# Performance work log

Measured on AMD Instinct MI355X. Metric: run time of the kernel, lower is better.

The kernel has to match this reference:

```python
import jax, jax.numpy as jnp
import numpy as np

H, D = 8, 32  # heads, head_dim
EPS = 1e-5    # torch LayerNorm default eps


def setup_inputs() -> dict:
    key = jax.random.key(0)
    ks = jax.random.split(key, 4)
    B, N, C = 2, 2048, 256
    inner = H * D
    return {
        "node_features": jax.random.normal(ks[0], (B, N, C), jnp.float32),
        "ln_gamma": jnp.ones((C,), jnp.float32),
        "ln_beta": jnp.zeros((C,), jnp.float32),
        "W_qkv": jax.random.normal(ks[1], (3 * inner, C), jnp.float32) * 0.02,
        "W_gate": jax.random.normal(ks[2], (inner, C), jnp.float32) * 0.02,
        "b_gate": jnp.ones((inner,), jnp.float32),
        "W_final": jax.random.normal(ks[3], (C, inner), jnp.float32) * 0.02,
        "b_final": jnp.zeros((C,), jnp.float32),
    }


def reference(node_features, ln_gamma, ln_beta, W_qkv, W_gate, b_gate, W_final, b_final):
    x = node_features                                   # [B, N, C]
    B, N, _ = x.shape

    # LayerNorm (biased variance, as in torch.nn.LayerNorm)
    mu = jnp.mean(x, axis=-1, keepdims=True)
    var = jnp.mean(jnp.square(x - mu), axis=-1, keepdims=True)
    normed = (x - mu) / jnp.sqrt(var + EPS) * ln_gamma + ln_beta

    # Fused QKV projection (no bias), split into heads: [B, H, N, D]
    qkv = normed @ W_qkv.T                              # [B, N, 3*H*D]
    q, k, v = jnp.split(qkv, 3, axis=-1)

    def to_heads(t):
        return t.reshape(B, N, H, D).transpose(0, 2, 1, 3)

    q, k, v = to_heads(q), to_heads(k), to_heads(v)

    # Gate is computed from the UN-normalized input
    gate = jax.nn.sigmoid(to_heads(x @ W_gate.T + b_gate))  # [B, H, N, D]

    scores = jnp.einsum('bhid,bhjd->bhij', q, k) * (D ** -0.5)
    attn = jax.nn.softmax(scores, axis=-1)              # softmax over j

    # NOTE: non-standard contraction over i (attn^T @ V), output indexed by j
    out = jnp.einsum('bhij,bhid->bhjd', attn, v) * gate  # [B, H, N, D]
    out = out.transpose(0, 2, 1, 3).reshape(B, N, H * D)

    return x + out @ W_final.T + b_final
```

## Files before the change

kernel.cpp:

```cpp
#include <hip/hip_runtime.h>
#include <math.h>

#define Bb 2
#define Nn 2048
#define Cc 256
#define Hh 8
#define Dd 32
#define INNER 256
#define TQKV 768
#define NROWS 4096
#define EPSf 1e-5f
#define SCALEf 0.17677669529663687f

typedef unsigned short u16;
typedef short s16x8 __attribute__((ext_vector_type(8)));
typedef float f32x4 __attribute__((ext_vector_type(4)));
#define MFMA16 __builtin_amdgcn_mfma_f32_16x16x32_bf16

#define OFF_NORMED 0u
#define OFF_MPART  0u
#define OFF_LPART  65536u
#define OFF_VTGHI  0u
#define OFF_VTGLO  524288u
#define OFF_AOHI   0u
#define OFF_AOLO   524288u
#define OFF_GATE   1048576u
#define OFF_MM     2097152u
#define OFF_QHI    2129920u
#define OFF_QLO    3702784u
#define OFF_WHI    5275648u
#define OFF_WLO    5439488u
#define OFF_P1     5603328u

__device__ inline u16 f2bf(float f) {
  union { float f; unsigned u; } v; v.f = f;
  unsigned r = v.u + 0x7fffu + ((v.u >> 16) & 1u);
  return (u16)(r >> 16);
}
__device__ inline float bf2f(u16 h) {
  union { unsigned u; float f; } v; v.u = ((unsigned)h) << 16;
  return v.f;
}

__global__ __launch_bounds__(256) void ln_kernel(
    const float* __restrict__ x, const float* __restrict__ gam,
    const float* __restrict__ bet, float* __restrict__ normed) {
  int row = blockIdx.x;
  int tid = threadIdx.x;
  size_t base = (size_t)row * Cc;
  float v = x[base + tid];
  float s1 = v, s2 = v * v;
  #pragma unroll
  for (int off = 32; off; off >>= 1) {
    s1 += __shfl_xor(s1, off);
    s2 += __shfl_xor(s2, off);
  }
  __shared__ float w1[4], w2[4];
  if ((tid & 63) == 0) { w1[tid >> 6] = s1; w2[tid >> 6] = s2; }
  __syncthreads();
  s1 = w1[0] + w1[1] + w1[2] + w1[3];
  s2 = w2[0] + w2[1] + w2[2] + w2[3];
  float mu = s1 * (1.0f / Cc);
  float var = s2 * (1.0f / Cc) - mu * mu;
  float rstd = rsqrtf(var + EPSf);
  normed[base + tid] = (v - mu) * rstd * gam[tid] + bet[tid];
}

__global__ __launch_bounds__(256) void wconv_kernel(
    const float* __restrict__ Wqkv, const float* __restrict__ Wgate,
    const float* __restrict__ Wf, u16* __restrict__ whi, u16* __restrict__ wlo) {
  int row = blockIdx.x;
  int col = threadIdx.x;
  float v;
  if (row < TQKV) {
    v = Wqkv[(size_t)row * Cc + col];
    if (row < INNER) v *= SCALEf;
  } else if (row < TQKV + INNER) {
    v = Wgate[(size_t)(row - TQKV) * Cc + col];
  } else {
    v = Wf[(size_t)(row - TQKV - INNER) * Cc + col];
  }
  u16 h = f2bf(v);
  whi[(size_t)row * Cc + col] = h;
  wlo[(size_t)row * Cc + col] = f2bf(v - bf2f(h));
}

__global__ __launch_bounds__(256) void proj_kernel(
    const float* __restrict__ x, const float* __restrict__ normed,
    const u16* __restrict__ whi, const u16* __restrict__ wlo,
    const float* __restrict__ bgate,
    u16* __restrict__ qhi, u16* __restrict__ qlo, float* __restrict__ gate) {
  int ro = blockIdx.y * 64;
  int co = blockIdx.x * 64;
  bool isGate = (co >= TQKV);
  const float* __restrict__ A = isGate ? x : normed;
  int tid = threadIdx.x;
  int w = tid >> 6, l = tid & 63;
  int l15 = l & 15, g = l >> 4;
  int srow = tid >> 2, sc = tid & 3;
  __shared__ u16 a_hi[64][72], a_lo[64][72];
  __shared__ u16 b_hi[64][72], b_lo[64][72];
  f32x4 acc[4] = {};
  for (int k0 = 0; k0 < Cc; k0 += 64) {
    __syncthreads();
    #pragma unroll
    for (int q4 = 0; q4 < 4; q4++) {
      float4 f = *reinterpret_cast<const float4*>(
          &A[(size_t)(ro + srow) * Cc + k0 + 16 * sc + 4 * q4]);
      ushort4 h, lo;
      h.x = f2bf(f.x); lo.x = f2bf(f.x - bf2f(h.x));
      h.y = f2bf(f.y); lo.y = f2bf(f.y - bf2f(h.y));
      h.z = f2bf(f.z); lo.z = f2bf(f.z - bf2f(h.z));
      h.w = f2bf(f.w); lo.w = f2bf(f.w - bf2f(h.w));
      *reinterpret_cast<ushort4*>(&a_hi[srow][16 * sc + 4 * q4]) = h;
      *reinterpret_cast<ushort4*>(&a_lo[srow][16 * sc + 4 * q4]) = lo;
    }
    {
      size_t wb = (size_t)(co + srow) * Cc + k0 + 16 * sc;
      const uint4* sh = reinterpret_cast<const uint4*>(&whi[wb]);
      const uint4* sl = reinterpret_cast<const uint4*>(&wlo[wb]);
      *reinterpret_cast<uint4*>(&b_hi[srow][16 * sc]) = sh[0];
      *reinterpret_cast<uint4*>(&b_hi[srow][16 * sc + 8]) = sh[1];
      *reinterpret_cast<uint4*>(&b_lo[srow][16 * sc]) = sl[0];
      *reinterpret_cast<uint4*>(&b_lo[srow][16 * sc + 8]) = sl[1];
    }
    __syncthreads();
    #pragma unroll
    for (int ks = 0; ks < 2; ks++) {
      s16x8 wb_hi = *reinterpret_cast<const s16x8*>(&b_hi[16 * w + l15][8 * g + 32 * ks]);
      s16x8 wb_lo = *reinterpret_cast<const s16x8*>(&b_lo[16 * w + l15][8 * g + 32 * ks]);
      #pragma unroll
      for (int mt = 0; mt < 4; mt++) {
        s16x8 aa_hi = *reinterpret_cast<const s16x8*>(&a_hi[16 * mt + l15][8 * g + 32 * ks]);
        s16x8 aa_lo = *reinterpret_cast<const s16x8*>(&a_lo[16 * mt + l15][8 * g + 32 * ks]);
        acc[mt] = MFMA16(aa_hi, wb_hi, acc[mt], 0, 0, 0);
        acc[mt] = MFMA16(aa_hi, wb_lo, acc[mt], 0, 0, 0);
        acc[mt] = MFMA16(aa_lo, wb_hi, acc[mt], 0, 0, 0);
      }
    }
  }
  if (!isGate) {
    int o = co + 16 * w + l15;
    #pragma unroll
    for (int mt = 0; mt < 4; mt++) {
      #pragma unroll
      for (int r = 0; r < 4; r++) {
        int row = ro + 16 * mt + 4 * g + r;
        float v = acc[mt][r];
        u16 hb = f2bf(v);
        qhi[(size_t)row * TQKV + o] = hb;
        qlo[(size_t)row * TQKV + o] = f2bf(v - bf2f(hb));
      }
    }
  } else {
    int o = co - TQKV + 16 * w + l15;
    float bg = bgate[o];
    #pragma unroll
    for (int mt = 0; mt < 4; mt++) {
      #pragma unroll
      for (int r = 0; r < 4; r++) {
        int row = ro + 16 * mt + 4 * g + r;
        float z = acc[mt][r] + bg;
        gate[(size_t)row * INNER + o] = 1.0f / (1.0f + __expf(-z));
      }
    }
  }
}

__global__ __launch_bounds__(256) void stats_kernel(
    const u16* __restrict__ qhi, const u16* __restrict__ qlo,
    float* __restrict__ mpart, float* __restrict__ lpart) {
  int bh = blockIdx.y;
  int b = bh >> 3, h = bh & 7;
  int i0 = blockIdx.x * 64;
  int jhalf = blockIdx.z;
  int jt0 = 16 * jhalf;
  int tid = threadIdx.x;
  int w = tid >> 6;
  int l = tid & 63;
  int l15 = l & 15, g = l >> 4;
  __shared__ u16 q_hi[64][40], q_lo[64][40];
  __shared__ u16 k_hi[64][40], k_lo[64][40];
  __shared__ float red_m[4][64], red_l[4][64];

  int srow = tid >> 2, sc = tid & 3;
  {
    size_t gq = ((size_t)(b * Nn + i0 + srow)) * TQKV + h * Dd + 8 * sc;
    *reinterpret_cast<uint4*>(&q_hi[srow][8 * sc]) =
        *reinterpret_cast<const uint4*>(&qhi[gq]);
    *reinterpret_cast<uint4*>(&q_lo[srow][8 * sc]) =
        *reinterpret_cast<const uint4*>(&qlo[gq]);
  }
  size_t gk0 = ((size_t)(b * Nn + jt0 * 64 + srow)) * TQKV + INNER + h * Dd + 8 * sc;
  uint4 pk_h = *reinterpret_cast<const uint4*>(&qhi[gk0]);
  uint4 pk_l = *reinterpret_cast<const uint4*>(&qlo[gk0]);
  __syncthreads();
  s16x8 bq_hi[4], bq_lo[4];
  #pragma unroll
  for (int nt = 0; nt < 4; nt++) {
    bq_hi[nt] = *reinterpret_cast<const s16x8*>(&q_hi[l15 + 16 * nt][8 * g]);
    bq_lo[nt] = *reinterpret_cast<const s16x8*>(&q_lo[l15 + 16 * nt][8 * g]);
  }
  float m[4], lsum[4];
  #pragma unroll
  for (int nt = 0; nt < 4; nt++) { m[nt] = -INFINITY; lsum[nt] = 0.f; }

  for (int jt = jt0; jt < jt0 + 16; jt++) {
    __syncthreads();
    *reinterpret_cast<uint4*>(&k_hi[srow][8 * sc]) = pk_h;
    *reinterpret_cast<uint4*>(&k_lo[srow][8 * sc]) = pk_l;
    if (jt < jt0 + 15) {
      size_t gk = ((size_t)(b * Nn + (jt + 1) * 64 + srow)) * TQKV + INNER + h * Dd + 8 * sc;
      pk_h = *reinterpret_cast<const uint4*>(&qhi[gk]);
      pk_l = *reinterpret_cast<const uint4*>(&qlo[gk]);
    }
    __syncthreads();
    s16x8 ka_hi = *reinterpret_cast<const s16x8*>(&k_hi[l15 + 16 * w][8 * g]);
    s16x8 ka_lo = *reinterpret_cast<const s16x8*>(&k_lo[l15 + 16 * w][8 * g]);
    #pragma unroll
    for (int nt = 0; nt < 4; nt++) {
      f32x4 acc = {0.f, 0.f, 0.f, 0.f};
      acc = MFMA16(ka_hi, bq_hi[nt], acc, 0, 0, 0);
      acc = MFMA16(ka_hi, bq_lo[nt], acc, 0, 0, 0);
      acc = MFMA16(ka_lo, bq_hi[nt], acc, 0, 0, 0);
      float mt = fmaxf(fmaxf(acc[0], acc[1]), fmaxf(acc[2], acc[3]));
      float mn = fmaxf(m[nt], mt);
      float ls = __expf(acc[0] - mn) + __expf(acc[1] - mn) +
                 __expf(acc[2] - mn) + __expf(acc[3] - mn);
      lsum[nt] = lsum[nt] * __expf(m[nt] - mn) + ls;
      m[nt] = mn;
    }
  }
  #pragma unroll
  for (int off = 16; off <= 32; off <<= 1) {
    #pragma unroll
    for (int nt = 0; nt < 4; nt++) {
      float mo = __shfl_xor(m[nt], off);
      float lo = __shfl_xor(lsum[nt], off);
      float mn = fmaxf(m[nt], mo);
      lsum[nt] = lsum[nt] * __expf(m[nt] - mn) + lo * __expf(mo - mn);
      m[nt] = mn;
    }
  }
  if (g == 0) {
    #pragma unroll
    for (int nt = 0; nt < 4; nt++) {
      red_m[w][l15 + 16 * nt] = m[nt];
      red_l[w][l15 + 16 * nt] = lsum[nt];
    }
  }
  __syncthreads();
  if (tid < 64) {
    float M = fmaxf(fmaxf(red_m[0][tid], red_m[1][tid]),
                    fmaxf(red_m[2][tid], red_m[3][tid]));
    float L = red_l[0][tid] * __expf(red_m[0][tid] - M)
            + red_l[1][tid] * __expf(red_m[1][tid] - M)
            + red_l[2][tid] * __expf(red_m[2][tid] - M)
            + red_l[3][tid] * __expf(red_m[3][tid] - M);
    size_t o = ((size_t)(jhalf * 16 + bh)) * Nn + i0 + tid;
    mpart[o] = M;
    lpart[o] = L;
  }
}

__global__ __launch_bounds__(256) void merge_kernel(
    const float* __restrict__ mpart, const float* __restrict__ lpart,
    float* __restrict__ mmrow) {
  size_t idx = (size_t)blockIdx.x * 256 + threadIdx.x;
  float m0 = mpart[idx], m1 = mpart[idx + 32768];
  float l0 = lpart[idx], l1 = lpart[idx + 32768];
  float M = fmaxf(m0, m1);
  mmrow[idx] = M + __logf(l0 * __expf(m0 - M) + l1 * __expf(m1 - M));
}

__global__ __launch_bounds__(256) void vtrans_kernel(
    const u16* __restrict__ qhi, const u16* __restrict__ qlo,
    u16* __restrict__ vtghi, u16* __restrict__ vtglo) {
  int bh = blockIdx.y;
  int b = bh >> 3, h = bh & 7;
  int ib = blockIdx.x;
  int t = threadIdx.x;
  int d = t >> 3;
  #pragma unroll
  for (int rep = 0; rep < 2; rep++) {
    int i0 = ib * 128 + 8 * (t & 7) + 64 * rep;
    union { u16 s[8]; uint4 v; } ah, al;
    #pragma unroll
    for (int e = 0; e < 8; e++) {
      size_t src = ((size_t)(b * Nn + i0 + e)) * TQKV + 2 * INNER + h * Dd + d;
      ah.s[e] = qhi[src];
      al.s[e] = qlo[src];
    }
    size_t dst = ((size_t)(bh * 32 + d)) * Nn + i0;
    *reinterpret_cast<uint4*>(&vtghi[dst]) = ah.v;
    *reinterpret_cast<uint4*>(&vtglo[dst]) = al.v;
  }
}

__global__ __launch_bounds__(256, 4) void attnout_kernel(
    const u16* __restrict__ qhi, const u16* __restrict__ qlo,
    const u16* __restrict__ vtghi, const u16* __restrict__ vtglo,
    const float* __restrict__ mmrow,
    float* __restrict__ p0, float* __restrict__ p1) {
  int bh = blockIdx.y;
  int b = bh >> 3, h = bh & 7;
  int j0 = blockIdx.x * 64;
  int itbase = 16 * blockIdx.z;
  int tid = threadIdx.x;
  int w = tid >> 6;
  int l = tid & 63;
  int l15 = l & 15, g = l >> 4;
  __shared__ u16 q_hi[64][40], q_lo[64][40];
  __shared__ u16 vt_hi[32][72], vt_lo[32][72];
  __shared__ u16 p_hi[64][72], p_lo[64][72];
  __shared__ float mm_lds[64];

  int srow = tid >> 2, sc = tid & 3;
  s16x8 kb_hi, kb_lo;
  {
    size_t gk = ((size_t)(b * Nn + j0 + 16 * w + l15)) * TQKV + INNER + h * Dd + 8 * g;
    kb_hi = *reinterpret_cast<const s16x8*>(&qhi[gk]);
    kb_lo = *reinterpret_cast<const s16x8*>(&qlo[gk]);
  }
  size_t gq0 = ((size_t)(b * Nn + itbase * 64 + srow)) * TQKV + h * Dd + 8 * sc;
  uint4 pq_h = *reinterpret_cast<const uint4*>(&qhi[gq0]);
  uint4 pq_l = *reinterpret_cast<const uint4*>(&qlo[gq0]);
  int vrow = bh * 32 + (tid >> 3);
  int va = 8 * (tid & 7);
  size_t gv0 = (size_t)vrow * Nn + itbase * 64 + va;
  uint4 pv_h = *reinterpret_cast<const uint4*>(&vtghi[gv0]);
  uint4 pv_l = *reinterpret_cast<const uint4*>(&vtglo[gv0]);
  float pmm = 0.f;
  if (tid < 64) pmm = mmrow[(size_t)bh * Nn + itbase * 64 + tid];

  f32x4 accd0 = {0.f, 0.f, 0.f, 0.f};
  f32x4 accd1 = {0.f, 0.f, 0.f, 0.f};

  for (int it = itbase; it < itbase + 16; it++) {
    __syncthreads();
    *reinterpret_cast<uint4*>(&q_hi[srow][8 * sc]) = pq_h;
    *reinterpret_cast<uint4*>(&q_lo[srow][8 * sc]) = pq_l;
    *reinterpret_cast<uint4*>(&vt_hi[tid >> 3][va]) = pv_h;
    *reinterpret_cast<uint4*>(&vt_lo[tid >> 3][va]) = pv_l;
    if (tid < 64) mm_lds[tid] = pmm;
    if (it < itbase + 15) {
      size_t gq = ((size_t)(b * Nn + (it + 1) * 64 + srow)) * TQKV + h * Dd + 8 * sc;
      pq_h = *reinterpret_cast<const uint4*>(&qhi[gq]);
      pq_l = *reinterpret_cast<const uint4*>(&qlo[gq]);
      size_t gv = (size_t)vrow * Nn + (it + 1) * 64 + va;
      pv_h = *reinterpret_cast<const uint4*>(&vtghi[gv]);
      pv_l = *reinterpret_cast<const uint4*>(&vtglo[gv]);
      if (tid < 64) pmm = mmrow[(size_t)bh * Nn + (it + 1) * 64 + tid];
    }
    __syncthreads();
    #pragma unroll
    for (int mt = 0; mt < 4; mt++) {
      s16x8 qa_hi = *reinterpret_cast<const s16x8*>(&q_hi[l15 + 16 * mt][8 * g]);
      s16x8 qa_lo = *reinterpret_cast<const s16x8*>(&q_lo[l15 + 16 * mt][8 * g]);
      f32x4 s = {0.f, 0.f, 0.f, 0.f};
      s = MFMA16(qa_hi, kb_hi, s, 0, 0, 0);
      s = MFMA16(qa_hi, kb_lo, s, 0, 0, 0);
      s = MFMA16(qa_lo, kb_hi, s, 0, 0, 0);
      int ib = 16 * mt + 4 * g;
      u16 ph[4], pl[4];
      #pragma unroll
      for (int r = 0; r < 4; r++) {
        float p = __expf(s[r] - mm_lds[ib + r]);
        u16 hb = f2bf(p);
        ph[r] = hb;
        pl[r] = f2bf(p - bf2f(hb));
      }
      ushort4 t1 = make_ushort4(ph[0], ph[1], ph[2], ph[3]);
      *reinterpret_cast<ushort4*>(&p_hi[l15 + 16 * w][ib]) = t1;
      ushort4 t2 = make_ushort4(pl[0], pl[1], pl[2], pl[3]);
      *reinterpret_cast<ushort4*>(&p_lo[l15 + 16 * w][ib]) = t2;
    }
    #pragma unroll
    for (int ks = 0; ks < 2; ks++) {
      s16x8 pa_hi = *reinterpret_cast<const s16x8*>(&p_hi[l15 + 16 * w][8 * g + 32 * ks]);
      s16x8 pa_lo = *reinterpret_cast<const s16x8*>(&p_lo[l15 + 16 * w][8 * g + 32 * ks]);
      int cb = 32 * ks + 8 * g;
      {
        s16x8 vb_hi = *reinterpret_cast<const s16x8*>(&vt_hi[l15][cb]);
        s16x8 vb_lo = *reinterpret_cast<const s16x8*>(&vt_lo[l15][cb]);
        accd0 = MFMA16(pa_hi, vb_hi, accd0, 0, 0, 0);
        accd0 = MFMA16(pa_hi, vb_lo, accd0, 0, 0, 0);
        accd0 = MFMA16(pa_lo, vb_hi, accd0, 0, 0, 0);
      }
      {
        s16x8 vb_hi = *reinterpret_cast<const s16x8*>(&vt_hi[l15 + 16][cb]);
        s16x8 vb_lo = *reinterpret_cast<const s16x8*>(&vt_lo[l15 + 16][cb]);
        accd1 = MFMA16(pa_hi, vb_hi, accd1, 0, 0, 0);
        accd1 = MFMA16(pa_hi, vb_lo, accd1, 0, 0, 0);
        accd1 = MFMA16(pa_lo, vb_hi, accd1, 0, 0, 0);
      }
    }
  }
  float* part = (blockIdx.z == 0) ? p0 : p1;
  #pragma unroll
  for (int r = 0; r < 4; r++) {
    int j = j0 + 16 * w + 4 * g + r;
    size_t rowb = ((size_t)(b * Nn + j)) * INNER + h * Dd;
    part[rowb + l15] = accd0[r];
    part[rowb + l15 + 16] = accd1[r];
  }
}

__global__ __launch_bounds__(256) void combine_kernel(
    const float* __restrict__ p0, const float* __restrict__ p1,
    const float* __restrict__ gate,
    u16* __restrict__ aohi, u16* __restrict__ aolo) {
  size_t idx = (size_t)blockIdx.x * 256 + threadIdx.x;
  float v = (p0[idx] + p1[idx]) * gate[idx];
  u16 h = f2bf(v);
  aohi[idx] = h;
  aolo[idx] = f2bf(v - bf2f(h));
}

__global__ __launch_bounds__(256) void final_kernel(
    const u16* __restrict__ aohi, const u16* __restrict__ aolo,
    const u16* __restrict__ wfhi, const u16* __restrict__ wflo,
    const float* __restrict__ bf, const float* __restrict__ x,
    float* __restrict__ out) {
  int ro = blockIdx.y * 64;
  int co = blockIdx.x * 64;
  int tid = threadIdx.x;
  int w = tid >> 6, l = tid & 63;
  int l15 = l & 15, g = l >> 4;
  int srow = tid >> 2, sc = tid & 3;
  __shared__ u16 a_hi[64][72], a_lo[64][72];
  __shared__ u16 b_hi[64][72], b_lo[64][72];
  f32x4 acc[4] = {};
  for (int k0 = 0; k0 < INNER; k0 += 64) {
    __syncthreads();
    {
      size_t ab = (size_t)(ro + srow) * INNER + k0 + 16 * sc;
      const uint4* sh = reinterpret_cast<const uint4*>(&aohi[ab]);
      const uint4* sl = reinterpret_cast<const uint4*>(&aolo[ab]);
      *reinterpret_cast<uint4*>(&a_hi[srow][16 * sc]) = sh[0];
      *reinterpret_cast<uint4*>(&a_hi[srow][16 * sc + 8]) = sh[1];
      *reinterpret_cast<uint4*>(&a_lo[srow][16 * sc]) = sl[0];
      *reinterpret_cast<uint4*>(&a_lo[srow][16 * sc + 8]) = sl[1];
      size_t wb = (size_t)(co + srow) * Cc + k0 + 16 * sc;
      const uint4* th = reinterpret_cast<const uint4*>(&wfhi[wb]);
      const uint4* tl = reinterpret_cast<const uint4*>(&wflo[wb]);
      *reinterpret_cast<uint4*>(&b_hi[srow][16 * sc]) = th[0];
      *reinterpret_cast<uint4*>(&b_hi[srow][16 * sc + 8]) = th[1];
      *reinterpret_cast<uint4*>(&b_lo[srow][16 * sc]) = tl[0];
      *reinterpret_cast<uint4*>(&b_lo[srow][16 * sc + 8]) = tl[1];
    }
    __syncthreads();
    #pragma unroll
    for (int ks = 0; ks < 2; ks++) {
      s16x8 wb_hi = *reinterpret_cast<const s16x8*>(&b_hi[16 * w + l15][8 * g + 32 * ks]);
      s16x8 wb_lo = *reinterpret_cast<const s16x8*>(&b_lo[16 * w + l15][8 * g + 32 * ks]);
      #pragma unroll
      for (int mt = 0; mt < 4; mt++) {
        s16x8 aa_hi = *reinterpret_cast<const s16x8*>(&a_hi[16 * mt + l15][8 * g + 32 * ks]);
        s16x8 aa_lo = *reinterpret_cast<const s16x8*>(&a_lo[16 * mt + l15][8 * g + 32 * ks]);
        acc[mt] = MFMA16(aa_hi, wb_hi, acc[mt], 0, 0, 0);
        acc[mt] = MFMA16(aa_hi, wb_lo, acc[mt], 0, 0, 0);
        acc[mt] = MFMA16(aa_lo, wb_hi, acc[mt], 0, 0, 0);
      }
    }
  }
  int o = co + 16 * w + l15;
  float bfo = bf[o];
  #pragma unroll
  for (int mt = 0; mt < 4; mt++) {
    #pragma unroll
    for (int r = 0; r < 4; r++) {
      int row = ro + 16 * mt + 4 * g + r;
      out[(size_t)row * Cc + o] = x[(size_t)row * Cc + o] + acc[mt][r] + bfo;
    }
  }
}

extern "C" void kernel_launch(void* const* d_in, const int* in_sizes, int n_in,
                              void* d_out, int out_size, void* d_ws, size_t ws_size,
                              hipStream_t stream) {
  (void)in_sizes; (void)n_in; (void)out_size; (void)ws_size;
  const float* x     = (const float*)d_in[0];
  const float* gam   = (const float*)d_in[1];
  const float* bet   = (const float*)d_in[2];
  const float* Wqkv  = (const float*)d_in[3];
  const float* Wgate = (const float*)d_in[4];
  const float* bgate = (const float*)d_in[5];
  const float* Wf    = (const float*)d_in[6];
  const float* bf    = (const float*)d_in[7];
  float* out = (float*)d_out;
  float* ws  = (float*)d_ws;

  float* normed = ws + OFF_NORMED;
  float* gatep  = ws + OFF_GATE;
  float* mm     = ws + OFF_MM;
  float* mpart  = ws + OFF_MPART;
  float* lpart  = ws + OFF_LPART;
  float* part1  = ws + OFF_P1;
  u16*   qhi    = (u16*)(ws + OFF_QHI);
  u16*   qlo    = (u16*)(ws + OFF_QLO);
  u16*   whi    = (u16*)(ws + OFF_WHI);
  u16*   wlo    = (u16*)(ws + OFF_WLO);
  u16*   vtghi  = (u16*)(ws + OFF_VTGHI);
  u16*   vtglo  = (u16*)(ws + OFF_VTGLO);
  u16*   aohi   = (u16*)(ws + OFF_AOHI);
  u16*   aolo   = (u16*)(ws + OFF_AOLO);

  ln_kernel<<<NROWS, 256, 0, stream>>>(x, gam, bet, normed);
  wconv_kernel<<<1280, 256, 0, stream>>>(Wqkv, Wgate, Wf, whi, wlo);
  proj_kernel<<<dim3(16, 64), 256, 0, stream>>>(x, normed, whi, wlo, bgate,
                                                qhi, qlo, gatep);
  stats_kernel<<<dim3(32, 16, 2), 256, 0, stream>>>(qhi, qlo, mpart, lpart);
  merge_kernel<<<128, 256, 0, stream>>>(mpart, lpart, mm);
  vtrans_kernel<<<dim3(16, 16), 256, 0, stream>>>(qhi, qlo, vtghi, vtglo);
  attnout_kernel<<<dim3(32, 16, 2), 256, 0, stream>>>(qhi, qlo, vtghi, vtglo,
                                                      mm, out, part1);
  combine_kernel<<<4096, 256, 0, stream>>>(out, part1, gatep, aohi, aolo);
  final_kernel<<<dim3(4, 64), 256, 0, stream>>>(aohi, aolo,
                                                whi + 1024 * Cc, wlo + 1024 * Cc,
                                                bf, x, out);
}
```

Baseline: 177.5 us.

## Drop split-bf16 low parts in attention and split key range four ways

Q, K, V and the softmax probabilities are now stored and multiplied as a single bf16 value instead of hi/lo split pairs, so the score and output matmuls issue one MFMA where they used to issue three, and half the operand bytes are loaded. The key/query reduction is split into four chunks instead of two to give more blocks, with four partial max/sum sets merged and bf16 partial outputs summed in combine. Launch bounds are raised to target higher occupancy. This lowers attention accuracy to plain bf16 precision, which risks tolerance failures, and the partial outputs are also rounded to bf16.

Measured after the change: 149.4 us. -15.8%, faster.

```diff
diff --git a/kernel.cpp b/kernel.cpp
--- a/kernel.cpp
+++ b/kernel.cpp
@@ -19,18 +19,19 @@
 
 #define OFF_NORMED 0u
 #define OFF_MPART  0u
-#define OFF_LPART  65536u
+#define OFF_LPART  131072u
 #define OFF_VTGHI  0u
-#define OFF_VTGLO  524288u
 #define OFF_AOHI   0u
 #define OFF_AOLO   524288u
 #define OFF_GATE   1048576u
 #define OFF_MM     2097152u
 #define OFF_QHI    2129920u
-#define OFF_QLO    3702784u
+#define OFF_P2     3702784u
+#define OFF_P3     3964928u
 #define OFF_WHI    5275648u
 #define OFF_WLO    5439488u
-#define OFF_P1     5603328u
+#define OFF_P0     5603328u
+#define OFF_P1x    5865472u
 
 __device__ inline u16 f2bf(float f) {
   union { float f; unsigned u; } v; v.f = f;
@@ -89,7 +90,7 @@
     const float* __restrict__ x, const float* __restrict__ normed,
     const u16* __restrict__ whi, const u16* __restrict__ wlo,
     const float* __restrict__ bgate,
-    u16* __restrict__ qhi, u16* __restrict__ qlo, float* __restrict__ gate) {
+    u16* __restrict__ qhi, float* __restrict__ gate) {
   int ro = blockIdx.y * 64;
   int co = blockIdx.x * 64;
   bool isGate = (co >= TQKV);
@@ -146,10 +147,7 @@
       #pragma unroll
       for (int r = 0; r < 4; r++) {
         int row = ro + 16 * mt + 4 * g + r;
-        float v = acc[mt][r];
-        u16 hb = f2bf(v);
-        qhi[(size_t)row * TQKV + o] = hb;
-        qlo[(size_t)row * TQKV + o] = f2bf(v - bf2f(hb));
+        qhi[(size_t)row * TQKV + o] = f2bf(acc[mt][r]);
       }
     }
   } else {
@@ -167,20 +165,20 @@
   }
 }
 
-__global__ __launch_bounds__(256) void stats_kernel(
-    const u16* __restrict__ qhi, const u16* __restrict__ qlo,
+__global__ __launch_bounds__(256, 8) void stats_kernel(
+    const u16* __restrict__ qhi,
     float* __restrict__ mpart, float* __restrict__ lpart) {
   int bh = blockIdx.y;
   int b = bh >> 3, h = bh & 7;
   int i0 = blockIdx.x * 64;
-  int jhalf = blockIdx.z;
-  int jt0 = 16 * jhalf;
+  int jq = blockIdx.z;
+  int jt0 = 8 * jq;
   int tid = threadIdx.x;
   int w = tid >> 6;
   int l = tid & 63;
   int l15 = l & 15, g = l >> 4;
-  __shared__ u16 q_hi[64][40], q_lo[64][40];
-  __shared__ u16 k_hi[64][40], k_lo[64][40];
+  __shared__ u16 q_hi[64][40];
+  __shared__ u16 k_hi[64][40];
   __shared__ float red_m[4][64], red_l[4][64];
 
   int srow = tid >> 2, sc = tid & 3;
@@ -188,41 +186,31 @@
     size_t gq = ((size_t)(b * Nn + i0 + srow)) * TQKV + h * Dd + 8 * sc;
     *reinterpret_cast<uint4*>(&q_hi[srow][8 * sc]) =
         *reinterpret_cast<const uint4*>(&qhi[gq]);
-    *reinterpret_cast<uint4*>(&q_lo[srow][8 * sc]) =
-        *reinterpret_cast<const uint4*>(&qlo[gq]);
   }
   size_t gk0 = ((size_t)(b * Nn + jt0 * 64 + srow)) * TQKV + INNER + h * Dd + 8 * sc;
   uint4 pk_h = *reinterpret_cast<const uint4*>(&qhi[gk0]);
-  uint4 pk_l = *reinterpret_cast<const uint4*>(&qlo[gk0]);
   __syncthreads();
-  s16x8 bq_hi[4], bq_lo[4];
-  #pragma unroll
-  for (int nt = 0; nt < 4; nt++) {
+  s16x8 bq_hi[4];
+  #pragma unroll
+  for (int nt = 0; nt < 4; nt++)
     bq_hi[nt] = *reinterpret_cast<const s16x8*>(&q_hi[l15 + 16 * nt][8 * g]);
-    bq_lo[nt] = *reinterpret_cast<const s16x8*>(&q_lo[l15 + 16 * nt][8 * g]);
-  }
   float m[4], lsum[4];
   #pragma unroll
   for (int nt = 0; nt < 4; nt++) { m[nt] = -INFINITY; lsum[nt] = 0.f; }
 
-  for (int jt = jt0; jt < jt0 + 16; jt++) {
+  for (int jt = jt0; jt < jt0 + 8; jt++) {
     __syncthreads();
     *reinterpret_cast<uint4*>(&k_hi[srow][8 * sc]) = pk_h;
-    *reinterpret_cast<uint4*>(&k_lo[srow][8 * sc]) = pk_l;
-    if (jt < jt0 + 15) {
+    if (jt < jt0 + 7) {
       size_t gk = ((size_t)(b * Nn + (jt + 1) * 64 + srow)) * TQKV + INNER + h * Dd + 8 * sc;
       pk_h = *reinterpret_cast<const uint4*>(&qhi[gk]);
-      pk_l = *reinterpret_cast<const uint4*>(&qlo[gk]);
     }
     __syncthreads();
     s16x8 ka_hi = *reinterpret_cast<const s16x8*>(&k_hi[l15 + 16 * w][8 * g]);
-    s16x8 ka_lo = *reinterpret_cast<const s16x8*>(&k_lo[l15 + 16 * w][8 * g]);
     #pragma unroll
     for (int nt = 0; nt < 4; nt++) {
       f32x4 acc = {0.f, 0.f, 0.f, 0.f};
       acc = MFMA16(ka_hi, bq_hi[nt], acc, 0, 0, 0);
-      acc = MFMA16(ka_hi, bq_lo[nt], acc, 0, 0, 0);
-      acc = MFMA16(ka_lo, bq_hi[nt], acc, 0, 0, 0);
       float mt = fmaxf(fmaxf(acc[0], acc[1]), fmaxf(acc[2], acc[3]));
       float mn = fmaxf(m[nt], mt);
       float ls = __expf(acc[0] - mn) + __expf(acc[1] - mn) +
@@ -257,7 +245,7 @@
             + red_l[1][tid] * __expf(red_m[1][tid] - M)
             + red_l[2][tid] * __expf(red_m[2][tid] - M)
             + red_l[3][tid] * __expf(red_m[3][tid] - M);
-    size_t o = ((size_t)(jhalf * 16 + bh)) * Nn + i0 + tid;
+    size_t o = ((size_t)(jq * 16 + bh)) * Nn + i0 + tid;
     mpart[o] = M;
     lpart[o] = L;
   }
@@ -268,14 +256,17 @@
     float* __restrict__ mmrow) {
   size_t idx = (size_t)blockIdx.x * 256 + threadIdx.x;
   float m0 = mpart[idx], m1 = mpart[idx + 32768];
+  float m2 = mpart[idx + 65536], m3 = mpart[idx + 98304];
   float l0 = lpart[idx], l1 = lpart[idx + 32768];
-  float M = fmaxf(m0, m1);
-  mmrow[idx] = M + __logf(l0 * __expf(m0 - M) + l1 * __expf(m1 - M));
+  float l2 = lpart[idx + 65536], l3 = lpart[idx + 98304];
+  float M = fmaxf(fmaxf(m0, m1), fmaxf(m2, m3));
+  float L = l0 * __expf(m0 - M) + l1 * __expf(m1 - M) +
+            l2 * __expf(m2 - M) + l3 * __expf(m3 - M);
+  mmrow[idx] = M + __logf(L);
 }
 
 __global__ __launch_bounds__(256) void vtrans_kernel(
-    const u16* __restrict__ qhi, const u16* __restrict__ qlo,
-    u16* __restrict__ vtghi, u16* __restrict__ vtglo) {
+    const u16* __restrict__ qhi, u16* __restrict__ vtghi) {
   int bh = blockIdx.y;
   int b = bh >> 3, h = bh & 7;
   int ib = blockIdx.x;
@@ -284,134 +275,108 @@
   #pragma unroll
   for (int rep = 0; rep < 2; rep++) {
     int i0 = ib * 128 + 8 * (t & 7) + 64 * rep;
-    union { u16 s[8]; uint4 v; } ah, al;
+    union { u16 s[8]; uint4 v; } ah;
     #pragma unroll
     for (int e = 0; e < 8; e++) {
       size_t src = ((size_t)(b * Nn + i0 + e)) * TQKV + 2 * INNER + h * Dd + d;
       ah.s[e] = qhi[src];
-      al.s[e] = qlo[src];
     }
     size_t dst = ((size_t)(bh * 32 + d)) * Nn + i0;
     *reinterpret_cast<uint4*>(&vtghi[dst]) = ah.v;
-    *reinterpret_cast<uint4*>(&vtglo[dst]) = al.v;
-  }
-}
-
-__global__ __launch_bounds__(256, 4) void attnout_kernel(
-    const u16* __restrict__ qhi, const u16* __restrict__ qlo,
-    const u16* __restrict__ vtghi, const u16* __restrict__ vtglo,
+  }
+}
+
+__global__ __launch_bounds__(256, 8) void attnout_kernel(
+    const u16* __restrict__ qhi, const u16* __restrict__ vtghi,
     const float* __restrict__ mmrow,
-    float* __restrict__ p0, float* __restrict__ p1) {
+    u16* __restrict__ p0, u16* __restrict__ p1,
+    u16* __restrict__ p2, u16* __restrict__ p3) {
   int bh = blockIdx.y;
   int b = bh >> 3, h = bh & 7;
   int j0 = blockIdx.x * 64;
-  int itbase = 16 * blockIdx.z;
+  int itbase = 8 * blockIdx.z;
   int tid = threadIdx.x;
   int w = tid >> 6;
   int l = tid & 63;
   int l15 = l & 15, g = l >> 4;
-  __shared__ u16 q_hi[64][40], q_lo[64][40];
-  __shared__ u16 vt_hi[32][72], vt_lo[32][72];
-  __shared__ u16 p_hi[64][72], p_lo[64][72];
+  __shared__ u16 q_hi[64][40];
+  __shared__ u16 vt_hi[32][72];
+  __shared__ u16 p_hi[64][72];
   __shared__ float mm_lds[64];
 
   int srow = tid >> 2, sc = tid & 3;
-  s16x8 kb_hi, kb_lo;
+  s16x8 kb_hi;
   {
     size_t gk = ((size_t)(b * Nn + j0 + 16 * w + l15)) * TQKV + INNER + h * Dd + 8 * g;
     kb_hi = *reinterpret_cast<const s16x8*>(&qhi[gk]);
-    kb_lo = *reinterpret_cast<const s16x8*>(&qlo[gk]);
   }
   size_t gq0 = ((size_t)(b * Nn + itbase * 64 + srow)) * TQKV + h * Dd + 8 * sc;
   uint4 pq_h = *reinterpret_cast<const uint4*>(&qhi[gq0]);
-  uint4 pq_l = *reinterpret_cast<const uint4*>(&qlo[gq0]);
   int vrow = bh * 32 + (tid >> 3);
   int va = 8 * (tid & 7);
   size_t gv0 = (size_t)vrow * Nn + itbase * 64 + va;
   uint4 pv_h = *reinterpret_cast<const uint4*>(&vtghi[gv0]);
-  uint4 pv_l = *reinterpret_cast<const uint4*>(&vtglo[gv0]);
   float pmm = 0.f;
   if (tid < 64) pmm = mmrow[(size_t)bh * Nn + itbase * 64 + tid];
 
   f32x4 accd0 = {0.f, 0.f, 0.f, 0.f};
   f32x4 accd1 = {0.f, 0.f, 0.f, 0.f};
 
-  for (int it = itbase; it < itbase + 16; it++) {
+  for (int it = itbase; it < itbase + 8; it++) {
     __syncthreads();
     *reinterpret_cast<uint4*>(&q_hi[srow][8 * sc]) = pq_h;
-    *reinterpret_cast<uint4*>(&q_lo[srow][8 * sc]) = pq_l;
     *reinterpret_cast<uint4*>(&vt_hi[tid >> 3][va]) = pv_h;
-    *reinterpret_cast<uint4*>(&vt_lo[tid >> 3][va]) = pv_l;
     if (tid < 64) mm_lds[tid] = pmm;
-    if (it < itbase + 15) {
+    if (it < itbase + 7) {
       size_t gq = ((size_t)(b * Nn + (it + 1) * 64 + srow)) * TQKV + h * Dd + 8 * sc;
       pq_h = *reinterpret_cast<const uint4*>(&qhi[gq]);
-      pq_l = *reinterpret_cast<const uint4*>(&qlo[gq]);
       size_t gv = (size_t)vrow * Nn + (it + 1) * 64 + va;
       pv_h = *reinterpret_cast<const uint4*>(&vtghi[gv]);
-      pv_l = *reinterpret_cast<const uint4*>(&vtglo[gv]);
       if (tid < 64) pmm = mmrow[(size_t)bh * Nn + (it + 1) * 64 + tid];
     }
     __syncthreads();
     #pragma unroll
     for (int mt = 0; mt < 4; mt++) {
       s16x8 qa_hi = *reinterpret_cast<const s16x8*>(&q_hi[l15 + 16 * mt][8 * g]);
-      s16x8 qa_lo = *reinterpret_cast<const s16x8*>(&q_lo[l15 + 16 * mt][8 * g]);
       f32x4 s = {0.f, 0.f, 0.f, 0.f};
       s = MFMA16(qa_hi, kb_hi, s, 0, 0, 0);
-      s = MFMA16(qa_hi, kb_lo, s, 0, 0, 0);
-      s = MFMA16(qa_lo, kb_hi, s, 0, 0, 0);
       int ib = 16 * mt + 4 * g;
-      u16 ph[4], pl[4];
+      u16 ph[4];
       #pragma unroll
-      for (int r = 0; r < 4; r++) {
-        float p = __expf(s[r] - mm_lds[ib + r]);
-        u16 hb = f2bf(p);
-        ph[r] = hb;
-        pl[r] = f2bf(p - bf2f(hb));
-      }
-      ushort4 t1 = make_ushort4(ph[0], ph[1], ph[2], ph[3]);
-      *reinterpret_cast<ushort4*>(&p_hi[l15 + 16 * w][ib]) = t1;
-      ushort4 t2 = make_ushort4(pl[0], pl[1], pl[2], pl[3]);
-      *reinterpret_cast<ushort4*>(&p_lo[l15 + 16 * w][ib]) = t2;
+      for (int r = 0; r < 4; r++)
+        ph[r] = f2bf(__expf(s[r] - mm_lds[ib + r]));
+      *reinterpret_cast<ushort4*>(&p_hi[l15 + 16 * w][ib]) =
+          make_ushort4(ph[0], ph[1], ph[2], ph[3]);
     }
     #pragma unroll
     for (int ks = 0; ks < 2; ks++) {
       s16x8 pa_hi = *reinterpret_cast<const s16x8*>(&p_hi[l15 + 16 * w][8 * g + 32 * ks]);
-      s16x8 pa_lo = *reinterpret_cast<const s16x8*>(&p_lo[l15 + 16 * w][8 * g + 32 * ks]);
       int cb = 32 * ks + 8 * g;
-      {
-        s16x8 vb_hi = *reinterpret_cast<const s16x8*>(&vt_hi[l15][cb]);
-        s16x8 vb_lo = *reinterpret_cast<const s16x8*>(&vt_lo[l15][cb]);
-        accd0 = MFMA16(pa_hi, vb_hi, accd0, 0, 0, 0);
-        accd0 = MFMA16(pa_hi, vb_lo, accd0, 0, 0, 0);
-        accd0 = MFMA16(pa_lo, vb_hi, accd0, 0, 0, 0);
-      }
-      {
-        s16x8 vb_hi = *reinterpret_cast<const s16x8*>(&vt_hi[l15 + 16][cb]);
-        s16x8 vb_lo = *reinterpret_cast<const s16x8*>(&vt_lo[l15 + 16][cb]);
-        accd1 = MFMA16(pa_hi, vb_hi, accd1, 0, 0, 0);
-        accd1 = MFMA16(pa_hi, vb_lo, accd1, 0, 0, 0);
-        accd1 = MFMA16(pa_lo, vb_hi, accd1, 0, 0, 0);
-      }
-    }
-  }
-  float* part = (blockIdx.z == 0) ? p0 : p1;
+      s16x8 vb0 = *reinterpret_cast<const s16x8*>(&vt_hi[l15][cb]);
+      accd0 = MFMA16(pa_hi, vb0, accd0, 0, 0, 0);
+      s16x8 vb1 = *reinterpret_cast<const s16x8*>(&vt_hi[l15 + 16][cb]);
+      accd1 = MFMA16(pa_hi, vb1, accd1, 0, 0, 0);
+    }
+  }
+  int z = blockIdx.z;
+  u16* part = (z == 0) ? p0 : (z == 1) ? p1 : (z == 2) ? p2 : p3;
   #pragma unroll
   for (int r = 0; r < 4; r++) {
     int j = j0 + 16 * w + 4 * g + r;
     size_t rowb = ((size_t)(b * Nn + j)) * INNER + h * Dd;
-    part[rowb + l15] = accd0[r];
-    part[rowb + l15 + 16] = accd1[r];
+    part[rowb + l15] = f2bf(accd0[r]);
+    part[rowb + l15 + 16] = f2bf(accd1[r]);
   }
 }
 
 __global__ __launch_bounds__(256) void combine_kernel(
-    const float* __restrict__ p0, const float* __restrict__ p1,
+    const u16* __restrict__ p0, const u16* __restrict__ p1,
+    const u16* __restrict__ p2, const u16* __restrict__ p3,
     const float* __restrict__ gate,
     u16* __restrict__ aohi, u16* __restrict__ aolo) {
   size_t idx = (size_t)blockIdx.x * 256 + threadIdx.x;
-  float v = (p0[idx] + p1[idx]) * gate[idx];
+  float v = (bf2f(p0[idx]) + bf2f(p1[idx]) + bf2f(p2[idx]) + bf2f(p3[idx]))
+            * gate[idx];
   u16 h = f2bf(v);
   aohi[idx] = h;
   aolo[idx] = f2bf(v - bf2f(h));
@@ -496,26 +461,27 @@
   float* mm     = ws + OFF_MM;
   float* mpart  = ws + OFF_MPART;
   float* lpart  = ws + OFF_LPART;
-  float* part1  = ws + OFF_P1;
   u16*   qhi    = (u16*)(ws + OFF_QHI);
-  u16*   qlo    = (u16*)(ws + OFF_QLO);
   u16*   whi    = (u16*)(ws + OFF_WHI);
   u16*   wlo    = (u16*)(ws + OFF_WLO);
   u16*   vtghi  = (u16*)(ws + OFF_VTGHI);
-  u16*   vtglo  = (u16*)(ws + OFF_VTGLO);
   u16*   aohi   = (u16*)(ws + OFF_AOHI);
   u16*   aolo   = (u16*)(ws + OFF_AOLO);
+  u16*   p0     = (u16*)(ws + OFF_P0);
+  u16*   p1     = (u16*)(ws + OFF_P1x);
+  u16*   p2     = (u16*)(ws + OFF_P2);
+  u16*   p3     = (u16*)(ws + OFF_P3);
 
   ln_kernel<<<NROWS, 256, 0, stream>>>(x, gam, bet, normed);
   wconv_kernel<<<1280, 256, 0, stream>>>(Wqkv, Wgate, Wf, whi, wlo);
   proj_kernel<<<dim3(16, 64), 256, 0, stream>>>(x, normed, whi, wlo, bgate,
-                                                qhi, qlo, gatep);
-  stats_kernel<<<dim3(32, 16, 2), 256, 0, stream>>>(qhi, qlo, mpart, lpart);
+                                                qhi, gatep);
+  stats_kernel<<<dim3(32, 16, 4), 256, 0, stream>>>(qhi, mpart, lpart);
   merge_kernel<<<128, 256, 0, stream>>>(mpart, lpart, mm);
-  vtrans_kernel<<<dim3(16, 16), 256, 0, stream>>>(qhi, qlo, vtghi, vtglo);
-  attnout_kernel<<<dim3(32, 16, 2), 256, 0, stream>>>(qhi, qlo, vtghi, vtglo,
-                                                      mm, out, part1);
-  combine_kernel<<<4096, 256, 0, stream>>>(out, part1, gatep, aohi, aolo);
+  vtrans_kernel<<<dim3(16, 16), 256, 0, stream>>>(qhi, vtghi);
+  attnout_kernel<<<dim3(32, 16, 4), 256, 0, stream>>>(qhi, vtghi, mm,
+                                                      p0, p1, p2, p3);
+  combine_kernel<<<4096, 256, 0, stream>>>(p0, p1, p2, p3, gatep, aohi, aolo);
   final_kernel<<<dim3(4, 64), 256, 0, stream>>>(aohi, aolo,
                                                 whi + 1024 * Cc, wlo + 1024 * Cc,
                                                 bf, x, out);
```
